# Kernel tuning notes

Measured on AMD Instinct MI355X. Metric: run time of the kernel, lower is better.

Reference implementation:

```python
import jax, jax.numpy as jnp
import numpy as np
import math


def setup_inputs() -> dict:
    key = jax.random.key(0)
    B, H, CL, QL = 16, 128, 2048, 256
    k0, k1, k2 = jax.random.split(key, 3)
    context = jax.random.normal(k0, (B, H, CL), dtype=jnp.float32)
    question = jax.random.normal(k1, (B, H, QL), dtype=jnp.float32)
    c_mask = jnp.ones((B, CL), dtype=jnp.int32)
    q_mask = jnp.ones((B, QL), dtype=jnp.int32)
    lim = math.sqrt(1.0 / H)
    w = jax.random.uniform(k2, (3 * H,), minval=-lim, maxval=lim, dtype=jnp.float32)
    return {"context": context, "question": question, "c_mask": c_mask, "q_mask": q_mask, "w": w}


def reference(context, question, c_mask, q_mask, w):
    # context: (B, H, c_len), question: (B, H, q_len), w: (3H,)
    H = context.shape[1]
    ctx = jnp.transpose(context, (0, 2, 1))   # (B, c_len, H)
    qry = jnp.transpose(question, (0, 2, 1))  # (B, q_len, H)
    wq, wc, wcq = w[:H], w[H:2 * H], w[2 * H:]
    # Trilinear similarity computed directly (no (B,c,q,3H) materialization):
    # s[b,i,j] = wq.q_j + wc.c_i + wcq.(c_i*q_j); torch layout after transpose is (B, c_len, q_len)
    s = (ctx @ wc)[:, :, None] + (qry @ wq)[:, None, :] + jnp.einsum('bch,bqh->bcq', ctx * wcq, qry)
    NEG = jnp.float32(-1e30)
    s1 = jax.nn.softmax(jnp.where(q_mask[:, None, :] > 0, s, NEG), axis=2)  # softmax over q
    s2 = jax.nn.softmax(jnp.where(c_mask[:, :, None] > 0, s, NEG), axis=1)  # softmax over c
    a = jnp.einsum('bcq,bqh->bch', s1, qry)          # context-to-query attention
    l = jnp.einsum('bcq,bkq->bck', s1, s2)           # s1 @ s2^T, (B, c_len, c_len)
    b = jnp.einsum('bck,bkh->bch', l, ctx)           # query-to-context attention
    out = jnp.concatenate([ctx, a, ctx * a, ctx * b], axis=2)  # (B, c_len, 4H)
    # drop_prob=0 -> dropout is identity
    return jnp.transpose(out, (0, 2, 1))  # (B, 4H, c_len)
```

## Files before the change

### kernel.cpp

```cpp
#include <hip/hip_runtime.h>

typedef short bf16x8 __attribute__((ext_vector_type(8)));
typedef float f32x16 __attribute__((ext_vector_type(16)));
typedef float f32x4  __attribute__((ext_vector_type(4)));
typedef unsigned int u32x4 __attribute__((ext_vector_type(4)));

constexpr int B  = 16;
constexpr int H  = 128;
constexpr int CL = 2048;
constexpr int QL = 256;
constexpr int SPLITK5 = 8;
constexpr int K5SEG = CL / SPLITK5;
constexpr float SHIFT = 8.0f;

__device__ __forceinline__ unsigned short f2bf(float x) {
  unsigned u = __float_as_uint(x);
  u += 0x7fffu + ((u >> 16) & 1u);
  return (unsigned short)(u >> 16);
}
__device__ __forceinline__ float bf2f(unsigned short u) {
  return __uint_as_float((unsigned)u << 16);
}

template<int L, bool SCALE, bool WOUT>
__device__ __forceinline__ void ktrans_body(
    const float* __restrict__ src, const float* __restrict__ wbias,
    const float* __restrict__ wscale,
    unsigned short* __restrict__ dlin, unsigned short* __restrict__ dT,
    float* __restrict__ pbias, float* __restrict__ outg0,
    int bxl, int h1, int b, int tid,
    unsigned short (*T)[72], float (*P)[64]) {
  const int c0 = bxl * 64;
  const int hh = tid >> 4;
  const int cc4 = (tid & 15) * 4;
  float4 part = make_float4(0.f, 0.f, 0.f, 0.f);
  #pragma unroll
  for (int it = 0; it < 4; ++it) {
    const int hrow = it * 16 + hh;
    const int h = h1 * 64 + hrow;
    float4 v = *(const float4*)&src[((size_t)b * H + h) * L + c0 + cc4];
    const float wb = wbias[h];
    part.x = fmaf(v.x, wb, part.x); part.y = fmaf(v.y, wb, part.y);
    part.z = fmaf(v.z, wb, part.z); part.w = fmaf(v.w, wb, part.w);
    if (WOUT) {
      f32x4 t;
      t[0] = v.x; t[1] = v.y; t[2] = v.z; t[3] = v.w;
      __builtin_nontemporal_store(
          t, (f32x4*)&outg0[((size_t)b * 4 * H + h) * (size_t)CL + c0 + cc4]);
    }
    ushort4 o;
    o.x = f2bf(v.x); o.y = f2bf(v.y); o.z = f2bf(v.z); o.w = f2bf(v.w);
    *(ushort4*)&dlin[((size_t)b * H + h) * L + c0 + cc4] = o;
    ushort4 ot;
    if (SCALE) {
      const float ws = wscale[h];
      ot.x = f2bf(v.x * ws); ot.y = f2bf(v.y * ws);
      ot.z = f2bf(v.z * ws); ot.w = f2bf(v.w * ws);
    } else {
      ot = o;
    }
    *(ushort4*)&T[hrow][cc4] = ot;
  }
  *(float4*)&P[hh][cc4] = part;
  __syncthreads();
  if (tid < 64) {
    float sum = 0.f;
    #pragma unroll
    for (int i = 0; i < 16; ++i) sum += P[i][tid];
    pbias[(size_t)h1 * B * L + (size_t)b * L + c0 + tid] = sum;
  }
  #pragma unroll
  for (int it = 0; it < 4; ++it) {
    int lin = it * 256 + tid;
    int c = lin >> 4, hc = (lin & 15) * 4;
    ushort4 o;
    o.x = T[hc + 0][c]; o.y = T[hc + 1][c];
    o.z = T[hc + 2][c]; o.w = T[hc + 3][c];
    *(ushort4*)&dT[((size_t)b * L + c0 + c) * H + h1 * 64 + hc] = o;
  }
}

__global__ __launch_bounds__(256) void ktrans_all(
    const float* __restrict__ ctx, const float* __restrict__ qry,
    const float* __restrict__ w,
    unsigned short* __restrict__ ctx_bf, unsigned short* __restrict__ ctxwT,
    unsigned short* __restrict__ qry_bf, unsigned short* __restrict__ qryT,
    float* __restrict__ pct, float* __restrict__ pqt,
    float* __restrict__ out) {
  __shared__ unsigned short T[64][72];
  __shared__ float P[16][64];
  const int h1 = blockIdx.y, b = blockIdx.z, tid = threadIdx.x;
  const int bx = blockIdx.x;
  if (bx < CL / 64) {
    ktrans_body<CL, true, true>(ctx, w + H, w + 2 * H, ctx_bf, ctxwT, pct, out,
                                bx, h1, b, tid, T, P);
  } else {
    ktrans_body<QL, false, false>(qry, w, w, qry_bf, qryT, pqt, nullptr,
                                  bx - CL / 64, h1, b, tid, T, P);
  }
}

__global__ __launch_bounds__(512) void k2_score5(
    const unsigned short* __restrict__ ctxwT, const unsigned short* __restrict__ qryT,
    const float* __restrict__ pct, const float* __restrict__ pqt,
    const int* __restrict__ cmask, const int* __restrict__ qmask,
    unsigned short* __restrict__ eu,
    float* __restrict__ rsum_g, float* __restrict__ Lpart) {
  __shared__ unsigned short t2[256 * 40];
  __shared__ float stats[32][8];
  __shared__ float cmf[32];
  const int wg = blockIdx.x;
  const int b = wg & (B - 1);
  const int cblk = wg >> 4;
  const int c0 = cblk * 32;
  const int tid = threadIdx.x;
  const int w = tid >> 6;
  const int l = tid & 63;
  const int lr = l & 31, hi = l >> 5;
  const int q0 = w * 32;
  const int c = c0 + lr;

  if (l < 32) cmf[l] = cmask[b * CL + c0 + l] > 0 ? 1.f : 0.f;

  const unsigned short* ap = qryT + ((size_t)b * QL + q0 + lr) * H + hi * 8;
  const unsigned short* bp = ctxwT + ((size_t)b * CL + c) * H + hi * 8;
  f32x16 acc = {};
  #pragma unroll
  for (int k = 0; k < H; k += 16) {
    bf16x8 af = *(const bf16x8*)(ap + k);
    bf16x8 bf_ = *(const bf16x8*)(bp + k);
    acc = __builtin_amdgcn_mfma_f32_32x32x16_bf16(af, bf_, acc, 0, 0, 0);
  }

  const float ct = pct[b * CL + c] + pct[B * CL + b * CL + c];

  float rs = 0.f;
  #pragma unroll
  for (int g = 0; g < 4; ++g) {
    const int qbase = q0 + 4 * hi + 8 * g;
    float4 qa = *(const float4*)&pqt[b * QL + qbase];
    float4 qb = *(const float4*)&pqt[B * QL + b * QL + qbase];
    int4 m4 = *(const int4*)&qmask[b * QL + qbase];
    float e0 = m4.x > 0 ? __expf(acc[4 * g + 0] + ct + qa.x + qb.x - SHIFT) : 0.f;
    float e1 = m4.y > 0 ? __expf(acc[4 * g + 1] + ct + qa.y + qb.y - SHIFT) : 0.f;
    float e2 = m4.z > 0 ? __expf(acc[4 * g + 2] + ct + qa.z + qb.z - SHIFT) : 0.f;
    float e3 = m4.w > 0 ? __expf(acc[4 * g + 3] + ct + qa.w + qb.w - SHIFT) : 0.f;
    rs += e0 + e1 + e2 + e3;
    t2[(qbase + 0) * 40 + lr] = f2bf(e0);
    t2[(qbase + 1) * 40 + lr] = f2bf(e1);
    t2[(qbase + 2) * 40 + lr] = f2bf(e2);
    t2[(qbase + 3) * 40 + lr] = f2bf(e3);
  }
  rs += __shfl_xor(rs, 32);
  if (hi == 0) stats[lr][w] = rs;

  __threadfence_block();
  {
    const int q = q0 + (l >> 1), co = (l & 1) * 16;
    bf16x8 v0 = *(const bf16x8*)&t2[q * 40 + co];
    bf16x8 v1 = *(const bf16x8*)&t2[q * 40 + co + 8];
    float cs = 0.f;
    #pragma unroll
    for (int i2 = 0; i2 < 8; ++i2) {
      cs += bf2f((unsigned short)v0[i2]) * cmf[co + i2];
      cs += bf2f((unsigned short)v1[i2]) * cmf[co + 8 + i2];
    }
    cs += __shfl_xor(cs, 1);
    unsigned short* op = eu + ((size_t)b * QL + q) * CL + c0 + co;
    *(bf16x8*)op = v0;
    *(bf16x8*)(op + 8) = v1;
    if ((l & 1) == 0) Lpart[((size_t)b * 64 + cblk) * QL + q] = cs;
  }
  __syncthreads();
  if (tid < 32) {
    float s = 0.f;
    #pragma unroll
    for (int ww = 0; ww < 8; ++ww) s += stats[tid][ww];
    rsum_g[b * CL + c0 + tid] = s;
  }
}

__global__ __launch_bounds__(256, 4) void k5_tpart(
    const unsigned short* __restrict__ eu,
    const unsigned short* __restrict__ ctxbf,
    const int* __restrict__ cmask,
    unsigned short* __restrict__ tpart) {
  __shared__ unsigned int cmm[K5SEG / 2];
  const int wg = blockIdx.x;
  const int b = wg & (B - 1);
  const int seg = (wg >> 4) & (SPLITK5 - 1);
  const int q0 = (wg >> 7) * 32;
  const int tid = threadIdx.x;
  if (tid < K5SEG / 2) {
    const int cbase = b * CL + seg * K5SEG + tid * 2;
    cmm[tid] = (cmask[cbase] > 0 ? 0xFFFFu : 0u) |
               (cmask[cbase + 1] > 0 ? 0xFFFF0000u : 0u);
  }
  __syncthreads();
  const int w = tid >> 6, l = tid & 63;
  const int h0 = w * 32;
  const int lr = l & 31, lg = l >> 5;
  const unsigned short* ap = eu + ((size_t)b * QL + q0 + lr) * CL + seg * K5SEG + lg * 8;
  const unsigned short* bp = ctxbf + ((size_t)b * H + h0 + lr) * CL + seg * K5SEG + lg * 8;
  f32x16 acc = {};
  #pragma unroll
  for (int k = 0; k < K5SEG; k += 16) {
    bf16x8 af = *(const bf16x8*)(ap + k);
    bf16x8 bfr = *(const bf16x8*)(bp + k);
    u32x4 mm = *(const u32x4*)&cmm[(k >> 1) + lg * 4];
    u32x4 ai = __builtin_bit_cast(u32x4, af);
    ai &= mm;
    af = __builtin_bit_cast(bf16x8, ai);
    acc = __builtin_amdgcn_mfma_f32_32x32x16_bf16(af, bfr, acc, 0, 0, 0);
  }
  unsigned short* tp = tpart + (size_t)(seg * B + b) * QL * H;
  #pragma unroll
  for (int r = 0; r < 16; ++r) {
    int qrow = (r & 3) + 8 * (r >> 2) + 4 * lg;
    tp[(size_t)(q0 + qrow) * H + h0 + lr] = f2bf(acc[r]);
  }
}

__global__ __launch_bounds__(256) void k5b_treduce(
    const unsigned short* __restrict__ tpart, const float* __restrict__ Lpart,
    unsigned short* __restrict__ tTbf) {
  __shared__ unsigned short lds[16 * 66];
  __shared__ float csum[4][64];
  __shared__ float cinv_s[64];
  const int q0 = blockIdx.x * 64, h0 = blockIdx.y * 16, b = blockIdx.z;
  const int tid = threadIdx.x;
  {
    const int qq = tid & 63, part = tid >> 6;
    float Ls = 0.f;
    #pragma unroll
    for (int k = 0; k < 16; ++k)
      Ls += Lpart[((size_t)b * 64 + part * 16 + k) * QL + q0 + qq];
    csum[part][qq] = Ls;
  }
  __syncthreads();
  if (tid < 64)
    cinv_s[tid] = 1.0f / (csum[0][tid] + csum[1][tid] + csum[2][tid] + csum[3][tid]);
  __syncthreads();
  for (int lin = tid; lin < 64 * 16; lin += 256) {
    int q = lin >> 4, h = lin & 15;
    float v = 0.f;
    #pragma unroll
    for (int sgt = 0; sgt < SPLITK5; ++sgt)
      v += bf2f(tpart[((size_t)(sgt * B + b) * QL + q0 + q) * H + h0 + h]);
    lds[h * 66 + q] = f2bf(v * cinv_s[q]);
  }
  __syncthreads();
  for (int lin = tid; lin < 16 * 64; lin += 256) {
    int h = lin >> 6, q = lin & 63;
    tTbf[((size_t)b * H + h0 + h) * QL + q0 + q] = lds[h * 66 + q];
  }
}

__device__ __forceinline__ int qswz(int q, int c) {
  return q ^ (((c >> 3) & 7) << 3);
}

__global__ __launch_bounds__(256) void kb_out(
    const unsigned short* __restrict__ eu,
    const unsigned short* __restrict__ qrybf, const unsigned short* __restrict__ tTbf,
    const unsigned short* __restrict__ ctxbf, const float* __restrict__ rsum_g,
    float* __restrict__ out) {
  __shared__ unsigned short Ps[32 * 264];
  const int wg = blockIdx.x;
  const int b = wg & (B - 1);
  const int c0 = (wg >> 4) * 32;
  const int tid = threadIdx.x;
  const int w = tid >> 6, l = tid & 63;
  const int lr = l & 31, hi = l >> 5;
  const int h0 = w * 32;
  const int c = c0 + lr;

  #pragma unroll
  for (int p = 0; p < 4; ++p) {
    const int lin = p * 256 + tid;
    const int q = lin >> 2, co8 = (lin & 3) * 8;
    bf16x8 v = *(const bf16x8*)&eu[((size_t)b * QL + q) * CL + c0 + co8];
    #pragma unroll
    for (int i = 0; i < 8; ++i) {
      const int cc = co8 + i;
      Ps[cc * 264 + qswz(q, cc)] = (unsigned short)v[i];
    }
  }

  const float rinv = 1.0f / rsum_g[b * CL + c];

  unsigned short cvu[16];
  {
    const unsigned short* cvp = ctxbf + (size_t)b * H * CL + c;
    #pragma unroll
    for (int r = 0; r < 16; ++r) {
      const int h = h0 + (r & 3) + 8 * (r >> 2) + 4 * hi;
      cvu[r] = cvp[(size_t)h * CL];
    }
  }
  __syncthreads();

  const unsigned short* a1p = qrybf + ((size_t)b * H + h0 + lr) * QL + hi * 8;
  const unsigned short* a2p = tTbf + ((size_t)b * H + h0 + lr) * QL + hi * 8;
  f32x16 accA = {}, accB = {};
  #pragma unroll
  for (int kc = 0; kc < 16; ++kc) {
    bf16x8 pb = *(const bf16x8*)&Ps[lr * 264 + qswz(kc * 16 + hi * 8, lr)];
    bf16x8 a1 = *(const bf16x8*)(a1p + kc * 16);
    bf16x8 a2 = *(const bf16x8*)(a2p + kc * 16);
    accA = __builtin_amdgcn_mfma_f32_32x32x16_bf16(a1, pb, accA, 0, 0, 0);
    accB = __builtin_amdgcn_mfma_f32_32x32x16_bf16(a2, pb, accB, 0, 0, 0);
  }
  float* ob = out + (size_t)b * 4 * H * CL;
  #pragma unroll
  for (int r = 0; r < 16; ++r) {
    const int h = h0 + (r & 3) + 8 * (r >> 2) + 4 * hi;
    const float cv = bf2f(cvu[r]);
    const float av = accA[r] * rinv;
    const float bv = accB[r] * rinv;
    __builtin_nontemporal_store(av, &ob[(size_t)(H + h) * CL + c]);
    __builtin_nontemporal_store(cv * av, &ob[(size_t)(2 * H + h) * CL + c]);
    __builtin_nontemporal_store(cv * bv, &ob[(size_t)(3 * H + h) * CL + c]);
  }
}

extern "C" void kernel_launch(void* const* d_in, const int* in_sizes, int n_in,
                              void* d_out, int out_size, void* d_ws, size_t ws_size,
                              hipStream_t stream) {
  const float* context  = (const float*)d_in[0];
  const float* question = (const float*)d_in[1];
  const int*   c_mask   = (const int*)d_in[2];
  const int*   q_mask   = (const int*)d_in[3];
  const float* w        = (const float*)d_in[4];
  float* out = (float*)d_out;

  char* ws = (char*)d_ws;
  size_t off = 0;
  auto alloc = [&](size_t bytes) -> void* {
    void* p = ws + off;
    off += (bytes + 255) & ~(size_t)255;
    return p;
  };
  unsigned short* ctx_bf = (unsigned short*)alloc((size_t)B * H * CL * 2);
  unsigned short* ctxwT  = (unsigned short*)alloc((size_t)B * CL * H * 2);
  unsigned short* qry_bf = (unsigned short*)alloc((size_t)B * H * QL * 2);
  unsigned short* qryT   = (unsigned short*)alloc((size_t)B * QL * H * 2);
  unsigned short* eu     = (unsigned short*)alloc((size_t)B * QL * CL * 2);
  unsigned short* tpart  = (unsigned short*)alloc((size_t)SPLITK5 * B * QL * H * 2);
  unsigned short* tT_bf  = (unsigned short*)alloc((size_t)B * H * QL * 2);
  float* pct   = (float*)alloc((size_t)2 * B * CL * sizeof(float));
  float* pqt   = (float*)alloc((size_t)2 * B * QL * sizeof(float));
  float* rsum_ = (float*)alloc((size_t)B * CL * sizeof(float));
  float* Lpart = (float*)alloc((size_t)B * 64 * QL * sizeof(float));

  ktrans_all<<<dim3(CL / 64 + QL / 64, H / 64, B), dim3(256), 0, stream>>>(
      context, question, w, ctx_bf, ctxwT, qry_bf, qryT, pct, pqt, out);

  k2_score5<<<dim3((CL / 32) * B), dim3(512), 0, stream>>>(
      ctxwT, qryT, pct, pqt, c_mask, q_mask, eu, rsum_, Lpart);

  k5_tpart<<<dim3((QL / 32) * SPLITK5 * B), dim3(256), 0, stream>>>(
      eu, ctx_bf, c_mask, tpart);

  k5b_treduce<<<dim3(QL / 64, H / 16, B), dim3(256), 0, stream>>>(
      tpart, Lpart, tT_bf);

  kb_out<<<dim3((CL / 32) * B), dim3(256), 0, stream>>>(
      eu, qry_bf, tT_bf, ctx_bf, rsum_, out);
}
```

Baseline: 85.68 us.

## Recompute score exponentials in consumers instead of materializing the eu matrix

Removes the separate score kernel and the bf16 exp-score buffer (B×QL×CL) that was written once and read twice. The tpart kernel now computes its own score tile with MFMA, applies the exponent into LDS and derives column sums itself. The output kernel recomputes the same scores per context block and takes row sums from LDS. This trades roughly doubled score-GEMM compute and exp work for one fewer launch and no large global write and reread.

Result: faster. 78.70 us (-8.1%).

```diff
diff --git a/kernel.cpp b/kernel.cpp
--- a/kernel.cpp
+++ b/kernel.cpp
@@ -3,7 +3,6 @@
 typedef short bf16x8 __attribute__((ext_vector_type(8)));
 typedef float f32x16 __attribute__((ext_vector_type(16)));
 typedef float f32x4  __attribute__((ext_vector_type(4)));
-typedef unsigned int u32x4 __attribute__((ext_vector_type(4)));
 
 constexpr int B  = 16;
 constexpr int H  = 128;
@@ -100,124 +99,87 @@
   }
 }
 
-__global__ __launch_bounds__(512) void k2_score5(
+__global__ __launch_bounds__(256) void k5_fused(
     const unsigned short* __restrict__ ctxwT, const unsigned short* __restrict__ qryT,
+    const unsigned short* __restrict__ ctxbf,
     const float* __restrict__ pct, const float* __restrict__ pqt,
-    const int* __restrict__ cmask, const int* __restrict__ qmask,
-    unsigned short* __restrict__ eu,
-    float* __restrict__ rsum_g, float* __restrict__ Lpart) {
-  __shared__ unsigned short t2[256 * 40];
-  __shared__ float stats[32][8];
-  __shared__ float cmf[32];
-  const int wg = blockIdx.x;
-  const int b = wg & (B - 1);
-  const int cblk = wg >> 4;
-  const int c0 = cblk * 32;
-  const int tid = threadIdx.x;
-  const int w = tid >> 6;
-  const int l = tid & 63;
-  const int lr = l & 31, hi = l >> 5;
-  const int q0 = w * 32;
-  const int c = c0 + lr;
-
-  if (l < 32) cmf[l] = cmask[b * CL + c0 + l] > 0 ? 1.f : 0.f;
-
-  const unsigned short* ap = qryT + ((size_t)b * QL + q0 + lr) * H + hi * 8;
-  const unsigned short* bp = ctxwT + ((size_t)b * CL + c) * H + hi * 8;
-  f32x16 acc = {};
-  #pragma unroll
-  for (int k = 0; k < H; k += 16) {
-    bf16x8 af = *(const bf16x8*)(ap + k);
-    bf16x8 bf_ = *(const bf16x8*)(bp + k);
-    acc = __builtin_amdgcn_mfma_f32_32x32x16_bf16(af, bf_, acc, 0, 0, 0);
-  }
-
-  const float ct = pct[b * CL + c] + pct[B * CL + b * CL + c];
-
-  float rs = 0.f;
-  #pragma unroll
-  for (int g = 0; g < 4; ++g) {
-    const int qbase = q0 + 4 * hi + 8 * g;
-    float4 qa = *(const float4*)&pqt[b * QL + qbase];
-    float4 qb = *(const float4*)&pqt[B * QL + b * QL + qbase];
-    int4 m4 = *(const int4*)&qmask[b * QL + qbase];
-    float e0 = m4.x > 0 ? __expf(acc[4 * g + 0] + ct + qa.x + qb.x - SHIFT) : 0.f;
-    float e1 = m4.y > 0 ? __expf(acc[4 * g + 1] + ct + qa.y + qb.y - SHIFT) : 0.f;
-    float e2 = m4.z > 0 ? __expf(acc[4 * g + 2] + ct + qa.z + qb.z - SHIFT) : 0.f;
-    float e3 = m4.w > 0 ? __expf(acc[4 * g + 3] + ct + qa.w + qb.w - SHIFT) : 0.f;
-    rs += e0 + e1 + e2 + e3;
-    t2[(qbase + 0) * 40 + lr] = f2bf(e0);
-    t2[(qbase + 1) * 40 + lr] = f2bf(e1);
-    t2[(qbase + 2) * 40 + lr] = f2bf(e2);
-    t2[(qbase + 3) * 40 + lr] = f2bf(e3);
-  }
-  rs += __shfl_xor(rs, 32);
-  if (hi == 0) stats[lr][w] = rs;
-
-  __threadfence_block();
-  {
-    const int q = q0 + (l >> 1), co = (l & 1) * 16;
-    bf16x8 v0 = *(const bf16x8*)&t2[q * 40 + co];
-    bf16x8 v1 = *(const bf16x8*)&t2[q * 40 + co + 8];
-    float cs = 0.f;
-    #pragma unroll
-    for (int i2 = 0; i2 < 8; ++i2) {
-      cs += bf2f((unsigned short)v0[i2]) * cmf[co + i2];
-      cs += bf2f((unsigned short)v1[i2]) * cmf[co + 8 + i2];
-    }
-    cs += __shfl_xor(cs, 1);
-    unsigned short* op = eu + ((size_t)b * QL + q) * CL + c0 + co;
-    *(bf16x8*)op = v0;
-    *(bf16x8*)(op + 8) = v1;
-    if ((l & 1) == 0) Lpart[((size_t)b * 64 + cblk) * QL + q] = cs;
-  }
-  __syncthreads();
-  if (tid < 32) {
-    float s = 0.f;
-    #pragma unroll
-    for (int ww = 0; ww < 8; ++ww) s += stats[tid][ww];
-    rsum_g[b * CL + c0 + tid] = s;
-  }
-}
-
-__global__ __launch_bounds__(256, 4) void k5_tpart(
-    const unsigned short* __restrict__ eu,
-    const unsigned short* __restrict__ ctxbf,
     const int* __restrict__ cmask,
-    unsigned short* __restrict__ tpart) {
-  __shared__ unsigned int cmm[K5SEG / 2];
+    unsigned short* __restrict__ tpart, float* __restrict__ Lpart) {
+  __shared__ unsigned short P[32 * 264];
   const int wg = blockIdx.x;
   const int b = wg & (B - 1);
   const int seg = (wg >> 4) & (SPLITK5 - 1);
   const int q0 = (wg >> 7) * 32;
+  const int cseg = seg * K5SEG;
   const int tid = threadIdx.x;
-  if (tid < K5SEG / 2) {
-    const int cbase = b * CL + seg * K5SEG + tid * 2;
-    cmm[tid] = (cmask[cbase] > 0 ? 0xFFFFu : 0u) |
-               (cmask[cbase + 1] > 0 ? 0xFFFF0000u : 0u);
-  }
-  __syncthreads();
   const int w = tid >> 6, l = tid & 63;
+  const int lr = l & 31, hi = l >> 5;
+
+  const unsigned short* ap = qryT + ((size_t)b * QL + q0 + lr) * H + hi * 8;
+  bf16x8 afr[8];
+  #pragma unroll
+  for (int k = 0; k < 8; ++k) afr[k] = *(const bf16x8*)(ap + k * 16);
+
+  #pragma unroll
+  for (int t2 = 0; t2 < 2; ++t2) {
+    const int cl = w * 64 + t2 * 32 + lr;
+    const int c = cseg + cl;
+    const unsigned short* bp = ctxwT + ((size_t)b * CL + c) * H + hi * 8;
+    f32x16 acc = {};
+    #pragma unroll
+    for (int k = 0; k < 8; ++k) {
+      bf16x8 bfr = *(const bf16x8*)(bp + k * 16);
+      acc = __builtin_amdgcn_mfma_f32_32x32x16_bf16(afr[k], bfr, acc, 0, 0, 0);
+    }
+    const float ct = pct[b * CL + c] + pct[B * CL + b * CL + c];
+    const bool cm = cmask[b * CL + c] > 0;
+    #pragma unroll
+    for (int g = 0; g < 4; ++g) {
+      const int ql = 4 * hi + 8 * g;
+      const int qbase = q0 + ql;
+      float4 qa = *(const float4*)&pqt[b * QL + qbase];
+      float4 qb = *(const float4*)&pqt[B * QL + b * QL + qbase];
+      const int key = (g & 3) << 3;
+      const int cs = cl ^ key;
+      P[(ql + 0) * 264 + cs] = f2bf(cm ? __expf(acc[4*g+0] + ct + qa.x + qb.x - SHIFT) : 0.f);
+      P[(ql + 1) * 264 + cs] = f2bf(cm ? __expf(acc[4*g+1] + ct + qa.y + qb.y - SHIFT) : 0.f);
+      P[(ql + 2) * 264 + cs] = f2bf(cm ? __expf(acc[4*g+2] + ct + qa.z + qb.z - SHIFT) : 0.f);
+      P[(ql + 3) * 264 + cs] = f2bf(cm ? __expf(acc[4*g+3] + ct + qa.w + qb.w - SHIFT) : 0.f);
+    }
+  }
+  __syncthreads();
+
   const int h0 = w * 32;
-  const int lr = l & 31, lg = l >> 5;
-  const unsigned short* ap = eu + ((size_t)b * QL + q0 + lr) * CL + seg * K5SEG + lg * 8;
-  const unsigned short* bp = ctxbf + ((size_t)b * H + h0 + lr) * CL + seg * K5SEG + lg * 8;
+  const unsigned short* bp2 = ctxbf + ((size_t)b * H + h0 + lr) * CL + cseg + hi * 8;
+  const int rkey = ((lr >> 3) & 3) << 3;
   f32x16 acc = {};
   #pragma unroll
-  for (int k = 0; k < K5SEG; k += 16) {
-    bf16x8 af = *(const bf16x8*)(ap + k);
-    bf16x8 bfr = *(const bf16x8*)(bp + k);
-    u32x4 mm = *(const u32x4*)&cmm[(k >> 1) + lg * 4];
-    u32x4 ai = __builtin_bit_cast(u32x4, af);
-    ai &= mm;
-    af = __builtin_bit_cast(bf16x8, ai);
+  for (int kc = 0; kc < 16; ++kc) {
+    bf16x8 af = *(const bf16x8*)&P[lr * 264 + ((kc * 16 + hi * 8) ^ rkey)];
+    bf16x8 bfr = *(const bf16x8*)(bp2 + kc * 16);
     acc = __builtin_amdgcn_mfma_f32_32x32x16_bf16(af, bfr, acc, 0, 0, 0);
   }
   unsigned short* tp = tpart + (size_t)(seg * B + b) * QL * H;
   #pragma unroll
   for (int r = 0; r < 16; ++r) {
-    int qrow = (r & 3) + 8 * (r >> 2) + 4 * lg;
+    int qrow = (r & 3) + 8 * (r >> 2) + 4 * hi;
     tp[(size_t)(q0 + qrow) * H + h0 + lr] = f2bf(acc[r]);
+  }
+
+  {
+    const int ql = tid >> 3, j = tid & 7;
+    const unsigned short* pr = &P[ql * 264 + j * 32];
+    float s = 0.f;
+    #pragma unroll
+    for (int k = 0; k < 4; ++k) {
+      bf16x8 v = *(const bf16x8*)(pr + k * 8);
+      #pragma unroll
+      for (int i = 0; i < 8; ++i) s += bf2f((unsigned short)v[i]);
+    }
+    s += __shfl_xor(s, 1);
+    s += __shfl_xor(s, 2);
+    s += __shfl_xor(s, 4);
+    if (j == 0) Lpart[((size_t)b * SPLITK5 + seg) * QL + q0 + ql] = s;
   }
 }
 
@@ -225,21 +187,16 @@
     const unsigned short* __restrict__ tpart, const float* __restrict__ Lpart,
     unsigned short* __restrict__ tTbf) {
   __shared__ unsigned short lds[16 * 66];
-  __shared__ float csum[4][64];
   __shared__ float cinv_s[64];
   const int q0 = blockIdx.x * 64, h0 = blockIdx.y * 16, b = blockIdx.z;
   const int tid = threadIdx.x;
-  {
-    const int qq = tid & 63, part = tid >> 6;
+  if (tid < 64) {
     float Ls = 0.f;
     #pragma unroll
-    for (int k = 0; k < 16; ++k)
-      Ls += Lpart[((size_t)b * 64 + part * 16 + k) * QL + q0 + qq];
-    csum[part][qq] = Ls;
-  }
-  __syncthreads();
-  if (tid < 64)
-    cinv_s[tid] = 1.0f / (csum[0][tid] + csum[1][tid] + csum[2][tid] + csum[3][tid]);
+    for (int s = 0; s < SPLITK5; ++s)
+      Ls += Lpart[((size_t)b * SPLITK5 + s) * QL + q0 + tid];
+    cinv_s[tid] = 1.0f / Ls;
+  }
   __syncthreads();
   for (int lin = tid; lin < 64 * 16; lin += 256) {
     int q = lin >> 4, h = lin & 15;
@@ -260,35 +217,60 @@
   return q ^ (((c >> 3) & 7) << 3);
 }
 
-__global__ __launch_bounds__(256) void kb_out(
-    const unsigned short* __restrict__ eu,
+__global__ __launch_bounds__(256) void kb_fused(
+    const unsigned short* __restrict__ ctxwT, const unsigned short* __restrict__ qryT,
     const unsigned short* __restrict__ qrybf, const unsigned short* __restrict__ tTbf,
-    const unsigned short* __restrict__ ctxbf, const float* __restrict__ rsum_g,
-    float* __restrict__ out) {
+    const unsigned short* __restrict__ ctxbf,
+    const float* __restrict__ pct, const float* __restrict__ pqt,
+    const int* __restrict__ qmask, float* __restrict__ out) {
   __shared__ unsigned short Ps[32 * 264];
+  __shared__ float stats[32][4];
   const int wg = blockIdx.x;
   const int b = wg & (B - 1);
   const int c0 = (wg >> 4) * 32;
   const int tid = threadIdx.x;
   const int w = tid >> 6, l = tid & 63;
   const int lr = l & 31, hi = l >> 5;
+  const int c = c0 + lr;
+
+  const unsigned short* bp = ctxwT + ((size_t)b * CL + c) * H + hi * 8;
+  bf16x8 bfr[8];
+  #pragma unroll
+  for (int k = 0; k < 8; ++k) bfr[k] = *(const bf16x8*)(bp + k * 16);
+
+  const float ct = pct[b * CL + c] + pct[B * CL + b * CL + c];
+
+  float rs = 0.f;
+  #pragma unroll
+  for (int t2 = 0; t2 < 2; ++t2) {
+    const int q0 = (2 * w + t2) * 32;
+    const unsigned short* ap = qryT + ((size_t)b * QL + q0 + lr) * H + hi * 8;
+    f32x16 acc = {};
+    #pragma unroll
+    for (int k = 0; k < 8; ++k)
+      acc = __builtin_amdgcn_mfma_f32_32x32x16_bf16(
+          *(const bf16x8*)(ap + k * 16), bfr[k], acc, 0, 0, 0);
+    #pragma unroll
+    for (int g = 0; g < 4; ++g) {
+      const int qbase = q0 + 4 * hi + 8 * g;
+      float4 qa = *(const float4*)&pqt[b * QL + qbase];
+      float4 qb = *(const float4*)&pqt[B * QL + b * QL + qbase];
+      int4 m4 = *(const int4*)&qmask[b * QL + qbase];
+      float e0 = m4.x > 0 ? __expf(acc[4*g+0] + ct + qa.x + qb.x - SHIFT) : 0.f;
+      float e1 = m4.y > 0 ? __expf(acc[4*g+1] + ct + qa.y + qb.y - SHIFT) : 0.f;
+      float e2 = m4.z > 0 ? __expf(acc[4*g+2] + ct + qa.z + qb.z - SHIFT) : 0.f;
+      float e3 = m4.w > 0 ? __expf(acc[4*g+3] + ct + qa.w + qb.w - SHIFT) : 0.f;
+      rs += e0 + e1 + e2 + e3;
+      const unsigned v01 = (unsigned)f2bf(e0) | ((unsigned)f2bf(e1) << 16);
+      const unsigned v23 = (unsigned)f2bf(e2) | ((unsigned)f2bf(e3) << 16);
+      *(unsigned*)&Ps[lr * 264 + qswz(qbase, lr)] = v01;
+      *(unsigned*)&Ps[lr * 264 + qswz(qbase + 2, lr)] = v23;
+    }
+  }
+  rs += __shfl_xor(rs, 32);
+  if (hi == 0) stats[lr][w] = rs;
+
   const int h0 = w * 32;
-  const int c = c0 + lr;
-
-  #pragma unroll
-  for (int p = 0; p < 4; ++p) {
-    const int lin = p * 256 + tid;
-    const int q = lin >> 2, co8 = (lin & 3) * 8;
-    bf16x8 v = *(const bf16x8*)&eu[((size_t)b * QL + q) * CL + c0 + co8];
-    #pragma unroll
-    for (int i = 0; i < 8; ++i) {
-      const int cc = co8 + i;
-      Ps[cc * 264 + qswz(q, cc)] = (unsigned short)v[i];
-    }
-  }
-
-  const float rinv = 1.0f / rsum_g[b * CL + c];
-
   unsigned short cvu[16];
   {
     const unsigned short* cvp = ctxbf + (size_t)b * H * CL + c;
@@ -299,6 +281,7 @@
     }
   }
   __syncthreads();
+  const float rinv = 1.0f / (stats[lr][0] + stats[lr][1] + stats[lr][2] + stats[lr][3]);
 
   const unsigned short* a1p = qrybf + ((size_t)b * H + h0 + lr) * QL + hi * 8;
   const unsigned short* a2p = tTbf + ((size_t)b * H + h0 + lr) * QL + hi * 8;
@@ -345,26 +328,21 @@
   unsigned short* ctxwT  = (unsigned short*)alloc((size_t)B * CL * H * 2);
   unsigned short* qry_bf = (unsigned short*)alloc((size_t)B * H * QL * 2);
   unsigned short* qryT   = (unsigned short*)alloc((size_t)B * QL * H * 2);
-  unsigned short* eu     = (unsigned short*)alloc((size_t)B * QL * CL * 2);
   unsigned short* tpart  = (unsigned short*)alloc((size_t)SPLITK5 * B * QL * H * 2);
   unsigned short* tT_bf  = (unsigned short*)alloc((size_t)B * H * QL * 2);
   float* pct   = (float*)alloc((size_t)2 * B * CL * sizeof(float));
   float* pqt   = (float*)alloc((size_t)2 * B * QL * sizeof(float));
-  float* rsum_ = (float*)alloc((size_t)B * CL * sizeof(float));
-  float* Lpart = (float*)alloc((size_t)B * 64 * QL * sizeof(float));
+  float* Lpart = (float*)alloc((size_t)B * SPLITK5 * QL * sizeof(float));
 
   ktrans_all<<<dim3(CL / 64 + QL / 64, H / 64, B), dim3(256), 0, stream>>>(
       context, question, w, ctx_bf, ctxwT, qry_bf, qryT, pct, pqt, out);
 
-  k2_score5<<<dim3((CL / 32) * B), dim3(512), 0, stream>>>(
-      ctxwT, qryT, pct, pqt, c_mask, q_mask, eu, rsum_, Lpart);
-
-  k5_tpart<<<dim3((QL / 32) * SPLITK5 * B), dim3(256), 0, stream>>>(
-      eu, ctx_bf, c_mask, tpart);
+  k5_fused<<<dim3((QL / 32) * SPLITK5 * B), dim3(256), 0, stream>>>(
+      ctxwT, qryT, ctx_bf, pct, pqt, c_mask, tpart, Lpart);
 
   k5b_treduce<<<dim3(QL / 64, H / 16, B), dim3(256), 0, stream>>>(
       tpart, Lpart, tT_bf);
 
-  kb_out<<<dim3((CL / 32) * B), dim3(256), 0, stream>>>(
-      eu, qry_bf, tT_bf, ctx_bf, rsum_, out);
-}
+  kb_fused<<<dim3((CL / 32) * B), dim3(256), 0, stream>>>(
+      ctxwT, qryT, qry_bf, tT_bf, ctx_bf, pct, pqt, q_mask, out);
+}
```
